# Optimization experiments

Measured on AMD Instinct MI355X. Metric: run time of the kernel, lower is better.

Reference implementation:

```python
import jax, jax.numpy as jnp
import numpy as np

K_NEIGHBORS = 50
DELTA = 0.001


def setup_inputs() -> dict:
    key = jax.random.key(0)
    k1, k2, k3 = jax.random.split(key, 3)
    A, N, D, B = 8, 50000, 64, 256
    return {
        "query": jax.random.normal(k1, (B, D), dtype=jnp.float32),
        "mem_keys": jax.random.normal(k2, (A, N, D), dtype=jnp.float32),
        "mem_values": jax.random.normal(k3, (A, N), dtype=jnp.float32),
    }


def reference(query, mem_keys, mem_values):
    # query: [B, D]; mem_keys: [A, N, D]; mem_values: [A, N]
    q_sq = jnp.sum(query ** 2, axis=-1, keepdims=True)  # [B, 1]

    def per_action(keys, values):
        # keys: [N, D], values: [N]
        # brute-force squared-L2 distances (replaces Annoy ANN search)
        d2 = q_sq + jnp.sum(keys ** 2, axis=-1)[None, :] - 2.0 * query @ keys.T  # [B, N]
        _, idx = jax.lax.top_k(-d2, K_NEIGHBORS)  # [B, K] nearest indices
        gk = keys[idx]        # [B, K, D] gathered keys
        gv = values[idx]      # [B, K]    gathered values
        # inverse-distance kernel, exact recompute as in torch forward
        dist = jnp.sum((query[:, None, :] - gk) ** 2, axis=-1)  # [B, K]
        w = 1.0 / (dist + DELTA)
        out = jnp.sum(w * gv, axis=-1) / jnp.sum(w, axis=-1)  # [B]
        return out, idx, dist

    vals, idxs, scores = jax.vmap(per_action)(mem_keys, mem_values)  # [A,B], [A,B,K], [A,B,K]
    values_all = vals.T  # [B, A]
    max_values = jnp.max(values_all, axis=-1, keepdims=True)   # [B, 1]
    actions = jnp.argmax(values_all, axis=-1, keepdims=True)   # [B, 1]
    return (max_values, actions, values_all,
            jnp.transpose(idxs, (1, 0, 2)), jnp.transpose(scores, (1, 0, 2)))
```

## Files before the change

kernel.cpp:

```cpp
#include <hip/hip_runtime.h>
#include <cstdint>


#define A_N 8
#define N_N 50000
#define D_N 64
#define B_N 256
#define K_N 50

constexpr int   QT  = 64;
constexpr int   NBT = 128;
constexpr int   NT  = (N_N + NBT - 1) / NBT;
constexpr int   NB64  = 64;
constexpr int   NT64  = 782;
constexpr int   SL64  = 64;
constexpr int   SLF = 64;
constexpr int   SLOTS = 12;
constexpr int   CAPMAX = 4096;
constexpr float TMARG = 25.0f;
constexpr int   NPAD = NT * NBT;

constexpr int OFF_MAX = 0;
constexpr int OFF_ACT = 256;
constexpr int OFF_VAL = 512;
constexpr int OFF_IDX = 2560;
constexpr int OFF_SC  = 104960;

constexpr size_t WSF_CNT  = 0;
constexpr size_t WSF_THR  = 8192;
constexpr size_t WSF_KBF  = 1609728;
constexpr size_t WSF_CAND = 52858880;

constexpr size_t WS_CNT  = 0;
constexpr size_t WS_QSQ  = 16384;
constexpr size_t WS_KSQ  = 17408;
constexpr size_t WS_CAND = 1617920;

typedef __attribute__((ext_vector_type(8))) short bf16x8;
typedef __attribute__((ext_vector_type(4))) float f32x4;

__device__ __forceinline__ unsigned bfr(float f)
{
    unsigned u = __float_as_uint(f);
    return (u + 0x7FFFu + ((u >> 16) & 1u)) >> 16;
}
__device__ __forceinline__ uint4 packbf8(const float* f)
{
    uint4 w;
    w.x = bfr(f[0]) | (bfr(f[1]) << 16);
    w.y = bfr(f[2]) | (bfr(f[3]) << 16);
    w.z = bfr(f[4]) | (bfr(f[5]) << 16);
    w.w = bfr(f[6]) | (bfr(f[7]) << 16);
    return w;
}

__device__ __forceinline__ void async16(void* lds, const void* g)
{
    __builtin_amdgcn_global_load_lds(
        (const __attribute__((address_space(1))) void*)g,
        (__attribute__((address_space(3))) void*)lds, 16, 0, 0);
}

__device__ __forceinline__ float np_tree8(const float r[8])
{
    return __fadd_rn(__fadd_rn(__fadd_rn(r[0], r[1]), __fadd_rn(r[2], r[3])),
                     __fadd_rn(__fadd_rn(r[4], r[5]), __fadd_rn(r[6], r[7])));
}

__device__ __forceinline__ float np_sumsq64(const float* __restrict__ a)
{
    float r[8];
#pragma unroll
    for (int j = 0; j < 8; ++j) r[j] = __fmul_rn(a[j], a[j]);
    for (int i = 8; i < 64; i += 8)
#pragma unroll
        for (int j = 0; j < 8; ++j)
            r[j] = __fadd_rn(r[j], __fmul_rn(a[i + j], a[i + j]));
    return np_tree8(r);
}

__device__ __forceinline__ float np_sum50(const float* __restrict__ a)
{
    float r[8];
#pragma unroll
    for (int j = 0; j < 8; ++j) r[j] = a[j];
    for (int i = 8; i < 48; i += 8)
#pragma unroll
        for (int j = 0; j < 8; ++j) r[j] = __fadd_rn(r[j], a[i + j]);
    float res = np_tree8(r);
    res = __fadd_rn(res, a[48]);
    res = __fadd_rn(res, a[49]);
    return res;
}


__global__ __launch_bounds__(256)
void dnd_k0b(const float* __restrict__ keys, float* __restrict__ thrn,
             uint4* __restrict__ kbf, int* __restrict__ cnt)
{
    __shared__ float khalf[NBT][2];
    const int t   = blockIdx.x;
    const int a   = blockIdx.y;
    const int tid = threadIdx.x;
    const int r   = tid >> 1, h = tid & 1;

    int n = t * NBT + r; if (n > N_N - 1) n = N_N - 1;
    const float4* s4 = (const float4*)(keys + ((size_t)a * N_N + n) * D_N + h * 32);
    float4 fv[8];
#pragma unroll
    for (int i = 0; i < 8; ++i) fv[i] = s4[i];
    float ps = 0.f;
#pragma unroll
    for (int i = 0; i < 8; ++i)
        ps += fv[i].x * fv[i].x + fv[i].y * fv[i].y + fv[i].z * fv[i].z + fv[i].w * fv[i].w;
    khalf[r][h] = ps;

    const float* f = (const float*)fv;
    const int T  = (t << 1) + (r >> 6);
    const int rr = r & 63;
    const int s = rr >> 4, m = rr & 15;
    uint4* dst = kbf + ((size_t)(a * NT64 + T) * 8 + (s * 2 + h)) * 64;
#pragma unroll
    for (int g = 0; g < 4; ++g) dst[g * 16 + m] = packbf8(f + g * 8);

    __syncthreads();
    if (tid < NBT) {
        const int nn = t * NBT + tid;
        float thr = __builtin_huge_valf();
        if (nn < N_N) {
            const float ks = khalf[tid][0] + khalf[tid][1];
            thr = 0.5f * (ks - TMARG);
        }
        thrn[(size_t)a * NPAD + t * NBT + tid] = thr;
    }
    if (t == 0) cnt[a * B_N + tid] = 0;
}

__global__ __launch_bounds__(256, 8)
void dnd_k1(const float* __restrict__ query, const uint4* __restrict__ kbf,
            const float* __restrict__ thrn,
            int* __restrict__ cnt, unsigned* __restrict__ cand, int cap)
{
    __shared__ __align__(16) uint4 bfrag[2][8][64];
    __shared__ __align__(16) float thrs[2][NB64];
    __shared__ int      lcnt[QT];
    __shared__ unsigned lbuf[QT][SLOTS];

    const int a    = blockIdx.z;
    const int q0   = blockIdx.y * QT;
    const int sl   = blockIdx.x;
    const int tid  = threadIdx.x;
    const int lane = tid & 63;
    const int wave = tid >> 6;
    const int quad = lane >> 4;
    const int nl   = lane & 15;

    bf16x8 aA, aB;
    {
        const float* qb = query + (size_t)(q0 + wave * 16 + nl) * D_N + quad * 8;
        float f0[8], f1[8];
        *(float4*)(f0)     = *(const float4*)(qb);
        *(float4*)(f0 + 4) = *(const float4*)(qb + 4);
        *(float4*)(f1)     = *(const float4*)(qb + 32);
        *(float4*)(f1 + 4) = *(const float4*)(qb + 36);
        uint4 pa = packbf8(f0), pb = packbf8(f1);
        aA = *(bf16x8*)&pa;
        aB = *(bf16x8*)&pb;
    }
    if (lane < 16) lcnt[wave * 16 + lane] = 0;

    {
        const char* src = (const char*)(kbf + (size_t)(a * NT64 + sl) * 512);
        char* dst = (char*)&bfrag[0][0][0];
        async16(dst + tid * 16,        src + tid * 16);
        async16(dst + 4096 + tid * 16, src + 4096 + tid * 16);
        if (tid < 16)
            async16((char*)&thrs[0][0] + tid * 16,
                    (const char*)(thrn + (size_t)a * NPAD + (size_t)sl * NB64) + tid * 16);
    }

    int it = 0, cur = 0;
    for (int T = sl; T < NT64; T += SL64, ++it) {
        __syncthreads();

        const int Tn = T + SL64;
        if (Tn < NT64) {
            const char* src = (const char*)(kbf + (size_t)(a * NT64 + Tn) * 512);
            char* dst = (char*)&bfrag[cur ^ 1][0][0];
            async16(dst + tid * 16,        src + tid * 16);
            async16(dst + 4096 + tid * 16, src + 4096 + tid * 16);
            if (tid < 16)
                async16((char*)&thrs[cur ^ 1][0] + tid * 16,
                        (const char*)(thrn + (size_t)a * NPAD + (size_t)Tn * NB64) + tid * 16);
        }

        const int n0 = T * NB64;
#pragma unroll
        for (int s = 0; s < 4; ++s) {
            const bf16x8 b0 = ((const bf16x8*)bfrag[cur])[(s * 2 + 0) * 64 + lane];
            const bf16x8 b1 = ((const bf16x8*)bfrag[cur])[(s * 2 + 1) * 64 + lane];
            f32x4 c = {0.f, 0.f, 0.f, 0.f};
            c = __builtin_amdgcn_mfma_f32_16x16x32_bf16(aA, b0, c, 0, 0, 0);
            c = __builtin_amdgcn_mfma_f32_16x16x32_bf16(aB, b1, c, 0, 0, 0);

            const int   nn  = n0 + s * 16 + nl;
            const float thr = thrs[cur][s * 16 + nl];
#pragma unroll
            for (int r = 0; r < 4; ++r) {
                if (c[r] >= thr) {
                    const int bl = wave * 16 + quad * 4 + r;
                    const float d2rel = fmaf(-2.f, c[r], fmaf(2.f, thr, TMARG));
                    int qv = (int)fmaf(d2rel, 1000.f, 40000.f);
                    qv = qv < 0 ? 0 : (qv > 65535 ? 65535 : qv);
                    const unsigned entry = ((unsigned)qv << 16) | (unsigned)nn;
                    const int p = atomicAdd(&lcnt[bl], 1);
                    if (p < SLOTS) lbuf[bl][p] = entry;
                    else {
                        const int gb = a * B_N + q0 + bl;
                        const int gp = atomicAdd(&cnt[gb], 1);
                        if (gp < cap) cand[(size_t)gb * cap + gp] = entry;
                    }
                }
            }
        }

        const bool last = (T + SL64 >= NT64);
        if ((it & 3) == 3 || last) {
            if (lane < 16) {
                const int bl = wave * 16 + lane;
                int m = lcnt[bl];
                if (m > 0) {
                    lcnt[bl] = 0;
                    if (m > SLOTS) m = SLOTS;
                    const int gb = a * B_N + q0 + bl;
                    const int base = atomicAdd(&cnt[gb], m);
                    unsigned* dst = cand + (size_t)gb * cap;
                    for (int i = 0; i < m; ++i) {
                        const int p = base + i;
                        if (p < cap) dst[p] = lbuf[bl][i];
                    }
                }
            }
        }
        cur ^= 1;
    }
}

__global__ __launch_bounds__(256)
void dnd_k2(const float* __restrict__ query, const float* __restrict__ keys,
            const float* __restrict__ values,
            const int* __restrict__ cnt, const unsigned* __restrict__ cand, int cap,
            float* __restrict__ dout)
{
    __shared__ __align__(16) float qrow[D_N];
    __shared__ int   hist[256];
    __shared__ float sdf[512];
    __shared__ int   sn[512];
    __shared__ int   wn[K_N];
    __shared__ float wsc[K_N];
    __shared__ float wgv[K_N];
    __shared__ int   nsurv;
    __shared__ int   bstar;
    __shared__ float qsq_np;

    const int b   = blockIdx.x;
    const int a   = blockIdx.y;
    const int ab  = a * B_N + b;
    const int tid = threadIdx.x;

    if (tid < D_N) qrow[tid] = query[(size_t)b * D_N + tid];
    hist[tid & 255] = 0;
    if (tid == 0) nsurv = 0;
    if (tid < K_N) wn[tid] = 0;
    __syncthreads();
    if (tid == 0) qsq_np = np_sumsq64(qrow);
    __syncthreads();

    int c = cnt[ab]; if (c > cap) c = cap;
    const unsigned* base = cand + (size_t)ab * cap;

    for (int i = tid; i < c; i += 256) {
        int bin = (int)(base[i] >> 16) / 250;
        bin = bin > 255 ? 255 : bin;
        atomicAdd(&hist[bin], 1);
    }
    __syncthreads();
    if (tid == 0) {
        const int need = c < K_N ? c : K_N;
        int cum = 0, bs = 255;
        for (int i = 0; i < 256; ++i) { cum += hist[i]; if (cum >= need) { bs = i; break; } }
        bstar = bs;
    }
    __syncthreads();
    const int bs = bstar + 4;

    for (int i = tid; i < c; i += 256) {
        const unsigned e = base[i];
        int bin = (int)(e >> 16) / 250;
        bin = bin > 255 ? 255 : bin;
        if (bin <= bs) {
            int p = atomicAdd(&nsurv, 1);
            if (p < 512) sn[p] = (int)(e & 0xFFFFu);
        }
    }
    __syncthreads();
    int c2 = nsurv; if (c2 > 512) c2 = 512;

    const float qn = qsq_np;
    for (int i = tid; i < c2; i += 256) {
        const int n = sn[i];
        const float4* kr = (const float4*)(keys + ((size_t)a * N_N + n) * D_N);
        const float4* qr = (const float4*)qrow;
        float r[8];
#pragma unroll
        for (int j = 0; j < 8; ++j) r[j] = 0.f;
        float dot = 0.f;
#pragma unroll
        for (int cch = 0; cch < 16; ++cch) {
            float4 kk = kr[cch]; float4 qv = qr[cch];
            const int j0 = (cch & 1) * 4;
            if (cch < 2) {
                r[j0 + 0] = __fmul_rn(kk.x, kk.x);
                r[j0 + 1] = __fmul_rn(kk.y, kk.y);
                r[j0 + 2] = __fmul_rn(kk.z, kk.z);
                r[j0 + 3] = __fmul_rn(kk.w, kk.w);
            } else {
                r[j0 + 0] = __fadd_rn(r[j0 + 0], __fmul_rn(kk.x, kk.x));
                r[j0 + 1] = __fadd_rn(r[j0 + 1], __fmul_rn(kk.y, kk.y));
                r[j0 + 2] = __fadd_rn(r[j0 + 2], __fmul_rn(kk.z, kk.z));
                r[j0 + 3] = __fadd_rn(r[j0 + 3], __fmul_rn(kk.w, kk.w));
            }
            dot = __fmaf_rn(qv.x, kk.x, dot);
            dot = __fmaf_rn(qv.y, kk.y, dot);
            dot = __fmaf_rn(qv.z, kk.z, dot);
            dot = __fmaf_rn(qv.w, kk.w, dot);
        }
        const float ksq = np_tree8(r);
        sdf[i] = __fsub_rn(__fadd_rn(qn, ksq), __fmul_rn(2.0f, dot));
    }
    __syncthreads();

    for (int i = tid; i < c2; i += 256) {
        const float di = sdf[i]; const int ni = sn[i];
        int rank = 0;
        for (int j = 0; j < c2; ++j) {
            const float dj = sdf[j]; const int nj = sn[j];
            rank += (dj < di || (dj == di && nj < ni)) ? 1 : 0;
        }
        if (rank < K_N) wn[rank] = ni;
    }
    __syncthreads();

    if (tid < K_N) {
        const int n = wn[tid];
        const float* kr = keys + ((size_t)a * N_N + n) * D_N;
        float r[8];
#pragma unroll
        for (int j = 0; j < 8; ++j) {
            float d = __fsub_rn(qrow[j], kr[j]);
            r[j] = __fmul_rn(d, d);
        }
        for (int i = 8; i < 64; i += 8)
#pragma unroll
            for (int j = 0; j < 8; ++j) {
                float d = __fsub_rn(qrow[i + j], kr[i + j]);
                r[j] = __fadd_rn(r[j], __fmul_rn(d, d));
            }
        const float dist = np_tree8(r);
        wsc[tid] = dist;
        wgv[tid] = values[(size_t)a * N_N + n];
        dout[OFF_IDX + (size_t)(b * A_N + a) * K_N + tid] = (float)n;
        dout[OFF_SC  + (size_t)(b * A_N + a) * K_N + tid] = dist;
    }
    __syncthreads();

    if (tid == 0) {
        float w[K_N], wv[K_N];
#pragma unroll
        for (int k = 0; k < K_N; ++k) {
            w[k]  = __fdiv_rn(1.0f, __fadd_rn(wsc[k], 0.001f));
            wv[k] = __fmul_rn(w[k], wgv[k]);
        }
        dout[OFF_VAL + b * A_N + a] = __fdiv_rn(np_sum50(wv), np_sum50(w));
    }
}

__global__ void dnd_k3(float* __restrict__ dout)
{
    const int b = threadIdx.x;
    float best = -__builtin_huge_valf(); int bi = 0;
#pragma unroll
    for (int a = 0; a < A_N; ++a) {
        const float v = dout[OFF_VAL + b * A_N + a];
        if (v > best) { best = v; bi = a; }
    }
    dout[OFF_MAX + b] = best;
    dout[OFF_ACT + b] = (float)bi;
}


__global__ __launch_bounds__(256)
void dnd_k0f(const float* __restrict__ query, const float* __restrict__ keys,
             float* __restrict__ qsq_g, float* __restrict__ ksq_g)
{
    const int r = blockIdx.x * 256 + threadIdx.x;
    if (r >= A_N * N_N + B_N) return;
    const bool isk = r < A_N * N_N;
    const float4* s4 = (const float4*)(isk ? (keys + (size_t)r * D_N)
                                           : (query + (size_t)(r - A_N * N_N) * D_N));
    float s = 0.f;
#pragma unroll
    for (int i = 0; i < 16; ++i) {
        float4 v = s4[i];
        s += v.x * v.x + v.y * v.y + v.z * v.z + v.w * v.w;
    }
    if (isk) ksq_g[r] = s; else qsq_g[r - A_N * N_N] = s;
}

__global__ __launch_bounds__(256, 4)
void dnd_k1f(const float* __restrict__ query, const float* __restrict__ keys,
             const float* __restrict__ qsq_g, const float* __restrict__ ksq_g,
             int* __restrict__ cnt, uint2* __restrict__ cand, int cap)
{
    __shared__ __align__(16) uint4 afrag[4][2][64];
    __shared__ __align__(16) uint4 bfrag[8][2][64];
    __shared__ float qsqs[QT];
    __shared__ float ksqs[NBT];

    const int a    = blockIdx.z;
    const int q0   = blockIdx.y * QT;
    const int sl   = blockIdx.x;
    const int tid  = threadIdx.x;
    const int lane = tid & 63;
    const int wave = tid >> 6;
    const int quad = lane >> 4;
    const int nl   = lane & 15;

    {
        const int r = tid & 63, seg = tid >> 6;
        const float4* s4 = (const float4*)(query + (size_t)(q0 + r) * D_N + seg * 16);
        float4 fv[4];
#pragma unroll
        for (int i = 0; i < 4; ++i) fv[i] = s4[i];
        const float* f = (const float*)fv;
        const int qtile = r >> 4, m = r & 15, kh = seg >> 1;
        const int quadA = (seg & 1) * 2;
        afrag[qtile][kh][quadA * 16 + m]       = packbf8(f);
        afrag[qtile][kh][(quadA + 1) * 16 + m] = packbf8(f + 8);
    }
    if (tid < QT) qsqs[tid] = qsq_g[q0 + tid];

    for (int t = sl; t < NT; t += SLF) {
        const int n0 = t * NBT;
        __syncthreads();
        {
            const int r = tid >> 1, h = tid & 1;
            int n = n0 + r; if (n > N_N - 1) n = N_N - 1;
            const float4* s4 = (const float4*)(keys + ((size_t)a * N_N + n) * D_N + h * 32);
            float4 fv[8];
#pragma unroll
            for (int i = 0; i < 8; ++i) fv[i] = s4[i];
            const float* f = (const float*)fv;
            const int s = r >> 4, m = r & 15;
#pragma unroll
            for (int g = 0; g < 4; ++g)
                bfrag[s][h][g * 16 + m] = packbf8(f + g * 8);
        }
        if (tid < NBT)
            ksqs[tid] = (n0 + tid < N_N) ? ksq_g[(size_t)a * N_N + n0 + tid]
                                         : __builtin_huge_valf();
        __syncthreads();

        const bf16x8 aA = ((const bf16x8*)afrag)[(wave * 2 + 0) * 64 + lane];
        const bf16x8 aB = ((const bf16x8*)afrag)[(wave * 2 + 1) * 64 + lane];

#pragma unroll
        for (int s = 0; s < 8; ++s) {
            const bf16x8 b0 = ((const bf16x8*)bfrag)[(s * 2 + 0) * 64 + lane];
            const bf16x8 b1 = ((const bf16x8*)bfrag)[(s * 2 + 1) * 64 + lane];
            f32x4 c = {0.f, 0.f, 0.f, 0.f};
            c = __builtin_amdgcn_mfma_f32_16x16x32_bf16(aA, b0, c, 0, 0, 0);
            c = __builtin_amdgcn_mfma_f32_16x16x32_bf16(aB, b1, c, 0, 0, 0);

            const int   nn  = n0 + s * 16 + nl;
            const float ksq = ksqs[s * 16 + nl];
#pragma unroll
            for (int r = 0; r < 4; ++r) {
                const int   qr = wave * 16 + quad * 4 + r;
                const float qq = qsqs[qr];
                const float d2 = qq + ksq - 2.0f * c[r];
                if (d2 <= qq + TMARG) {
                    const int b = q0 + qr;
                    const int p = atomicAdd(&cnt[a * B_N + b], 1);
                    if (p < cap) {
                        uint2 e; e.x = __float_as_uint(d2); e.y = (unsigned)nn;
                        cand[(size_t)(a * B_N + b) * cap + p] = e;
                    }
                }
            }
        }
    }
}

__global__ __launch_bounds__(256, 2)
void dnd_k2f(const float* __restrict__ query, const float* __restrict__ keys,
             const float* __restrict__ values,
             const int* __restrict__ cnt, const uint2* __restrict__ cand, int cap,
             float* __restrict__ dout)
{
    __shared__ __align__(16) float qrow[D_N];
    __shared__ float cd[CAPMAX];
    __shared__ int   cn[CAPMAX];
    __shared__ int   hist[256];
    __shared__ float sdf[512];
    __shared__ int   sn[512];
    __shared__ int   wn[K_N];
    __shared__ float wsc[K_N];
    __shared__ float wgv[K_N];
    __shared__ int   nsurv;
    __shared__ int   bstar;
    __shared__ float sqsq;
    __shared__ float qsq_np;

    const int b   = blockIdx.x;
    const int a   = blockIdx.y;
    const int ab  = a * B_N + b;
    const int tid = threadIdx.x;

    if (tid < D_N) qrow[tid] = query[(size_t)b * D_N + tid];
    hist[tid & 255] = 0;
    if (tid == 0) nsurv = 0;
    if (tid < K_N) wn[tid] = 0;
    __syncthreads();
    if (tid < 64) {
        float v = qrow[tid];
        float s = v * v;
#pragma unroll
        for (int m = 1; m < 64; m <<= 1) s += __shfl_xor(s, m, 64);
        if (tid == 0) sqsq = s;
    }
    if (tid == 0) qsq_np = np_sumsq64(qrow);
    __syncthreads();

    int c = cnt[ab]; if (c > cap) c = cap; if (c > CAPMAX) c = CAPMAX;
    const float qq = sqsq;

    for (int i = tid; i < c; i += 256) {
        uint2 e = cand[(size_t)ab * cap + i];
        float d = __uint_as_float(e.x);
        cd[i] = d; cn[i] = (int)e.y;
        int bin = (int)((d - qq + 40.f) * 4.f);
        bin = bin < 0 ? 0 : (bin > 255 ? 255 : bin);
        atomicAdd(&hist[bin], 1);
    }
    __syncthreads();
    if (tid == 0) {
        const int need = c < K_N ? c : K_N;
        int cum = 0, bs = 255;
        for (int i = 0; i < 256; ++i) { cum += hist[i]; if (cum >= need) { bs = i; break; } }
        bstar = bs;
    }
    __syncthreads();
    const int bs = bstar + 4;

    for (int i = tid; i < c; i += 256) {
        float d = cd[i];
        int bin = (int)((d - qq + 40.f) * 4.f);
        bin = bin < 0 ? 0 : (bin > 255 ? 255 : bin);
        if (bin <= bs) {
            int p = atomicAdd(&nsurv, 1);
            if (p < 512) sn[p] = cn[i];
        }
    }
    __syncthreads();
    int c2 = nsurv; if (c2 > 512) c2 = 512;

    const float qn = qsq_np;
    for (int i = tid; i < c2; i += 256) {
        const int n = sn[i];
        const float4* kr = (const float4*)(keys + ((size_t)a * N_N + n) * D_N);
        const float4* qr = (const float4*)qrow;
        float r[8];
#pragma unroll
        for (int j = 0; j < 8; ++j) r[j] = 0.f;
        float dot = 0.f;
#pragma unroll
        for (int cch = 0; cch < 16; ++cch) {
            float4 kk = kr[cch]; float4 qv = qr[cch];
            const int j0 = (cch & 1) * 4;
            if (cch < 2) {
                r[j0 + 0] = __fmul_rn(kk.x, kk.x);
                r[j0 + 1] = __fmul_rn(kk.y, kk.y);
                r[j0 + 2] = __fmul_rn(kk.z, kk.z);
                r[j0 + 3] = __fmul_rn(kk.w, kk.w);
            } else {
                r[j0 + 0] = __fadd_rn(r[j0 + 0], __fmul_rn(kk.x, kk.x));
                r[j0 + 1] = __fadd_rn(r[j0 + 1], __fmul_rn(kk.y, kk.y));
                r[j0 + 2] = __fadd_rn(r[j0 + 2], __fmul_rn(kk.z, kk.z));
                r[j0 + 3] = __fadd_rn(r[j0 + 3], __fmul_rn(kk.w, kk.w));
            }
            dot = __fmaf_rn(qv.x, kk.x, dot);
            dot = __fmaf_rn(qv.y, kk.y, dot);
            dot = __fmaf_rn(qv.z, kk.z, dot);
            dot = __fmaf_rn(qv.w, kk.w, dot);
        }
        const float ksq = np_tree8(r);
        sdf[i] = __fsub_rn(__fadd_rn(qn, ksq), __fmul_rn(2.0f, dot));
    }
    __syncthreads();

    for (int i = tid; i < c2; i += 256) {
        const float di = sdf[i]; const int ni = sn[i];
        int rank = 0;
        for (int j = 0; j < c2; ++j) {
            const float dj = sdf[j]; const int nj = sn[j];
            rank += (dj < di || (dj == di && nj < ni)) ? 1 : 0;
        }
        if (rank < K_N) wn[rank] = ni;
    }
    __syncthreads();

    if (tid < K_N) {
        const int n = wn[tid];
        const float* kr = keys + ((size_t)a * N_N + n) * D_N;
        float r[8];
#pragma unroll
        for (int j = 0; j < 8; ++j) {
            float d = __fsub_rn(qrow[j], kr[j]);
            r[j] = __fmul_rn(d, d);
        }
        for (int i = 8; i < 64; i += 8)
#pragma unroll
            for (int j = 0; j < 8; ++j) {
                float d = __fsub_rn(qrow[i + j], kr[i + j]);
                r[j] = __fadd_rn(r[j], __fmul_rn(d, d));
            }
        const float dist = np_tree8(r);
        wsc[tid] = dist;
        wgv[tid] = values[(size_t)a * N_N + n];
        dout[OFF_IDX + (size_t)(b * A_N + a) * K_N + tid] = (float)n;
        dout[OFF_SC  + (size_t)(b * A_N + a) * K_N + tid] = dist;
    }
    __syncthreads();

    if (tid == 0) {
        float w[K_N], wv[K_N];
#pragma unroll
        for (int k = 0; k < K_N; ++k) {
            w[k]  = __fdiv_rn(1.0f, __fadd_rn(wsc[k], 0.001f));
            wv[k] = __fmul_rn(w[k], wgv[k]);
        }
        dout[OFF_VAL + b * A_N + a] = __fdiv_rn(np_sum50(wv), np_sum50(w));
    }
}

extern "C" void kernel_launch(void* const* d_in, const int* in_sizes, int n_in,
                              void* d_out, int out_size, void* d_ws, size_t ws_size,
                              hipStream_t stream)
{
    (void)in_sizes; (void)n_in; (void)out_size;
    const float* query  = (const float*)d_in[0];
    const float* keys   = (const float*)d_in[1];
    const float* values = (const float*)d_in[2];
    float* dout = (float*)d_out;
    char*  ws   = (char*)d_ws;

    long long capf = 0;
    if (ws_size > WSF_CAND)
        capf = (long long)((ws_size - WSF_CAND) / ((size_t)A_N * B_N * 4));
    const bool full = capf >= 3072;

    if (full) {
        int cap = capf > CAPMAX ? CAPMAX : (int)capf;
        int*      cnt  = (int*)(ws + WSF_CNT);
        float*    thrn = (float*)(ws + WSF_THR);
        uint4*    kbf  = (uint4*)(ws + WSF_KBF);
        unsigned* cand = (unsigned*)(ws + WSF_CAND);

        dim3 g0(NT, A_N);
        dnd_k0b<<<g0, 256, 0, stream>>>(keys, thrn, kbf, cnt);
        dim3 g1(SL64, 4, A_N);
        dnd_k1<<<g1, 256, 0, stream>>>(query, kbf, thrn, cnt, cand, cap);
        dim3 g2(B_N, A_N);
        dnd_k2<<<g2, 256, 0, stream>>>(query, keys, values, cnt, cand, cap, dout);
        dnd_k3<<<1, 256, 0, stream>>>(dout);
    } else {
        int*   cnt   = (int*)(ws + WS_CNT);
        float* qsq_g = (float*)(ws + WS_QSQ);
        float* ksq_g = (float*)(ws + WS_KSQ);
        uint2* cand  = (uint2*)(ws + WS_CAND);
        int cap = CAPMAX;
        if (ws_size > WS_CAND) {
            size_t avail = (ws_size - WS_CAND) / ((size_t)A_N * B_N * 8);
            if ((size_t)cap > avail) cap = (int)avail;
        }
        if (cap < 1) cap = 1;

        hipMemsetAsync(cnt, 0, A_N * B_N * sizeof(int), stream);
        dnd_k0f<<<(A_N * N_N + B_N + 255) / 256, 256, 0, stream>>>(query, keys, qsq_g, ksq_g);
        dim3 g1(SLF, 4, A_N);
        dnd_k1f<<<g1, 256, 0, stream>>>(query, keys, qsq_g, ksq_g, cnt, cand, cap);
        dim3 g2(B_N, A_N);
        dnd_k2f<<<g2, 256, 0, stream>>>(query, keys, values, cnt, cand, cap, dout);
        dnd_k3<<<1, 256, 0, stream>>>(dout);
    }
}
```

Measured before the change: 268.6 us.

## Process 128 queries per block and load key fragments directly from global

```diff
diff --git a/kernel.cpp b/kernel.cpp
--- a/kernel.cpp
+++ b/kernel.cpp
@@ -13,7 +13,7 @@
 constexpr int   NT  = (N_N + NBT - 1) / NBT;
 constexpr int   NB64  = 64;
 constexpr int   NT64  = 782;
-constexpr int   SL64  = 64;
+constexpr int   SLQ   = 128;
 constexpr int   SLF = 64;
 constexpr int   SLOTS = 12;
 constexpr int   CAPMAX = 4096;
@@ -136,18 +136,16 @@
     if (t == 0) cnt[a * B_N + tid] = 0;
 }
 
-__global__ __launch_bounds__(256, 8)
+__global__ __launch_bounds__(256, 6)
 void dnd_k1(const float* __restrict__ query, const uint4* __restrict__ kbf,
             const float* __restrict__ thrn,
             int* __restrict__ cnt, unsigned* __restrict__ cand, int cap)
 {
-    __shared__ __align__(16) uint4 bfrag[2][8][64];
-    __shared__ __align__(16) float thrs[2][NB64];
-    __shared__ int      lcnt[QT];
-    __shared__ unsigned lbuf[QT][SLOTS];
+    __shared__ int      lcnt[128];
+    __shared__ unsigned lbuf[128][SLOTS];
 
     const int a    = blockIdx.z;
-    const int q0   = blockIdx.y * QT;
+    const int q0   = blockIdx.y * 128;
     const int sl   = blockIdx.x;
     const int tid  = threadIdx.x;
     const int lane = tid & 63;
@@ -155,79 +153,67 @@
     const int quad = lane >> 4;
     const int nl   = lane & 15;
 
-    bf16x8 aA, aB;
-    {
-        const float* qb = query + (size_t)(q0 + wave * 16 + nl) * D_N + quad * 8;
+    bf16x8 aF[2][2];
+#pragma unroll
+    for (int sub = 0; sub < 2; ++sub) {
+        const float* qb = query + (size_t)(q0 + (wave * 2 + sub) * 16 + nl) * D_N + quad * 8;
         float f0[8], f1[8];
         *(float4*)(f0)     = *(const float4*)(qb);
         *(float4*)(f0 + 4) = *(const float4*)(qb + 4);
         *(float4*)(f1)     = *(const float4*)(qb + 32);
         *(float4*)(f1 + 4) = *(const float4*)(qb + 36);
         uint4 pa = packbf8(f0), pb = packbf8(f1);
-        aA = *(bf16x8*)&pa;
-        aB = *(bf16x8*)&pb;
-    }
-    if (lane < 16) lcnt[wave * 16 + lane] = 0;
-
-    {
-        const char* src = (const char*)(kbf + (size_t)(a * NT64 + sl) * 512);
-        char* dst = (char*)&bfrag[0][0][0];
-        async16(dst + tid * 16,        src + tid * 16);
-        async16(dst + 4096 + tid * 16, src + 4096 + tid * 16);
-        if (tid < 16)
-            async16((char*)&thrs[0][0] + tid * 16,
-                    (const char*)(thrn + (size_t)a * NPAD + (size_t)sl * NB64) + tid * 16);
-    }
-
-    int it = 0, cur = 0;
-    for (int T = sl; T < NT64; T += SL64, ++it) {
-        __syncthreads();
-
-        const int Tn = T + SL64;
-        if (Tn < NT64) {
-            const char* src = (const char*)(kbf + (size_t)(a * NT64 + Tn) * 512);
-            char* dst = (char*)&bfrag[cur ^ 1][0][0];
-            async16(dst + tid * 16,        src + tid * 16);
-            async16(dst + 4096 + tid * 16, src + 4096 + tid * 16);
-            if (tid < 16)
-                async16((char*)&thrs[cur ^ 1][0] + tid * 16,
-                        (const char*)(thrn + (size_t)a * NPAD + (size_t)Tn * NB64) + tid * 16);
-        }
-
+        aF[sub][0] = *(bf16x8*)&pa;
+        aF[sub][1] = *(bf16x8*)&pb;
+    }
+    if (lane < 32) lcnt[wave * 32 + lane] = 0;
+
+    const uint4* kb_a = kbf + (size_t)a * NT64 * 512;
+    const float* th_a = thrn + (size_t)a * NPAD;
+
+    int it = 0;
+    for (int T = sl; T < NT64; T += SLQ, ++it) {
+        const uint4* tb = kb_a + (size_t)T * 512;
         const int n0 = T * NB64;
+
 #pragma unroll
         for (int s = 0; s < 4; ++s) {
-            const bf16x8 b0 = ((const bf16x8*)bfrag[cur])[(s * 2 + 0) * 64 + lane];
-            const bf16x8 b1 = ((const bf16x8*)bfrag[cur])[(s * 2 + 1) * 64 + lane];
-            f32x4 c = {0.f, 0.f, 0.f, 0.f};
-            c = __builtin_amdgcn_mfma_f32_16x16x32_bf16(aA, b0, c, 0, 0, 0);
-            c = __builtin_amdgcn_mfma_f32_16x16x32_bf16(aB, b1, c, 0, 0, 0);
-
+            const uint4 b0r = tb[(s * 2 + 0) * 64 + lane];
+            const uint4 b1r = tb[(s * 2 + 1) * 64 + lane];
+            const bf16x8 b0 = *(const bf16x8*)&b0r;
+            const bf16x8 b1 = *(const bf16x8*)&b1r;
             const int   nn  = n0 + s * 16 + nl;
-            const float thr = thrs[cur][s * 16 + nl];
-#pragma unroll
-            for (int r = 0; r < 4; ++r) {
-                if (c[r] >= thr) {
-                    const int bl = wave * 16 + quad * 4 + r;
-                    const float d2rel = fmaf(-2.f, c[r], fmaf(2.f, thr, TMARG));
-                    int qv = (int)fmaf(d2rel, 1000.f, 40000.f);
-                    qv = qv < 0 ? 0 : (qv > 65535 ? 65535 : qv);
-                    const unsigned entry = ((unsigned)qv << 16) | (unsigned)nn;
-                    const int p = atomicAdd(&lcnt[bl], 1);
-                    if (p < SLOTS) lbuf[bl][p] = entry;
-                    else {
-                        const int gb = a * B_N + q0 + bl;
-                        const int gp = atomicAdd(&cnt[gb], 1);
-                        if (gp < cap) cand[(size_t)gb * cap + gp] = entry;
+            const float thr = th_a[nn];
+
+#pragma unroll
+            for (int sub = 0; sub < 2; ++sub) {
+                f32x4 c = {0.f, 0.f, 0.f, 0.f};
+                c = __builtin_amdgcn_mfma_f32_16x16x32_bf16(aF[sub][0], b0, c, 0, 0, 0);
+                c = __builtin_amdgcn_mfma_f32_16x16x32_bf16(aF[sub][1], b1, c, 0, 0, 0);
+#pragma unroll
+                for (int r = 0; r < 4; ++r) {
+                    if (c[r] >= thr) {
+                        const int bl = (wave * 2 + sub) * 16 + quad * 4 + r;
+                        const float d2rel = fmaf(-2.f, c[r], fmaf(2.f, thr, TMARG));
+                        int qv = (int)fmaf(d2rel, 1000.f, 40000.f);
+                        qv = qv < 0 ? 0 : (qv > 65535 ? 65535 : qv);
+                        const unsigned entry = ((unsigned)qv << 16) | (unsigned)nn;
+                        const int p = atomicAdd(&lcnt[bl], 1);
+                        if (p < SLOTS) lbuf[bl][p] = entry;
+                        else {
+                            const int gb = a * B_N + q0 + bl;
+                            const int gp = atomicAdd(&cnt[gb], 1);
+                            if (gp < cap) cand[(size_t)gb * cap + gp] = entry;
+                        }
                     }
                 }
             }
         }
 
-        const bool last = (T + SL64 >= NT64);
+        const bool last = (T + SLQ >= NT64);
         if ((it & 3) == 3 || last) {
-            if (lane < 16) {
-                const int bl = wave * 16 + lane;
+            if (lane < 32) {
+                const int bl = wave * 32 + lane;
                 int m = lcnt[bl];
                 if (m > 0) {
                     lcnt[bl] = 0;
@@ -242,7 +228,6 @@
                 }
             }
         }
-        cur ^= 1;
     }
 }
 
@@ -679,7 +664,7 @@
 
         dim3 g0(NT, A_N);
         dnd_k0b<<<g0, 256, 0, stream>>>(keys, thrn, kbf, cnt);
-        dim3 g1(SL64, 4, A_N);
+        dim3 g1(SLQ, 2, A_N);
         dnd_k1<<<g1, 256, 0, stream>>>(query, kbf, thrn, cnt, cand, cap);
         dim3 g2(B_N, A_N);
         dnd_k2<<<g2, 256, 0, stream>>>(query, keys, values, cnt, cand, cap, dout);
```

Measured after the change: 282.6 us. 5.2% more time.
